# Kernel optimization log

Hardware: AMD Instinct MI355X
Metric: run time of the kernel (lower is better)

The kernel has to match this reference:

```python
import jax, jax.numpy as jnp
import numpy as np

B, N, D = 4096, 20, 256
MAX_STEPS = int(N * 1.5)  # exploration_ratio = 1.5


def setup_inputs() -> dict:
    key = jax.random.key(0)
    ks = jax.random.split(key, 9)
    s = 1.0 / np.sqrt(D)
    u = lambda k, shape: jax.random.uniform(k, shape, jnp.float32, -s, s)
    return {
        "node_emb": jax.random.normal(ks[0], (B, N, D), jnp.float32),
        "mask": jnp.ones((B, N), jnp.bool_),  # present in signature, unused by forward
        "W_ih": u(ks[1], (4 * D, D)),
        "W_hh": u(ks[2], (4 * D, D)),
        "b_ih": u(ks[3], (4 * D,)),
        "b_hh": u(ks[4], (4 * D,)),
        "attn_w": u(ks[5], (D, D)),
        "attn_b": u(ks[6], (D,)),
        "done_w": u(ks[7], (D,)),
        "done_b": u(ks[8], ()),
        "revisit_penalty": jnp.float32(-0.05),
        "greedy": 1,
    }


def reference(node_emb, mask, W_ih, W_hh, b_ih, b_hh, attn_w, attn_b, done_w, done_b, revisit_penalty, greedy):
    Bx, Nx, Dx = node_emb.shape
    aB = jnp.arange(Bx)
    aN = jnp.arange(Nx)
    scale = 1.0 / jnp.sqrt(jnp.float32(Dx))
    keys = node_emb @ attn_w.T + attn_b  # [B, N, D], loop-invariant

    def step(carry, t):
        h, c, inp, visited, unique, complete, first = carry
        # LSTMCell (PyTorch gate order i, f, g, o)
        gates = inp @ W_ih.T + b_ih + h @ W_hh.T + b_hh
        i, f, g, o = jnp.split(gates, 4, axis=1)
        c2 = jax.nn.sigmoid(f) * c + jax.nn.sigmoid(i) * jnp.tanh(g)
        h2 = jax.nn.sigmoid(o) * jnp.tanh(c2)
        # done predictor (greedy: complete when sigmoid > 0.5)
        done_p = jax.nn.sigmoid(h2 @ done_w + done_b)  # [B]
        eligible = (~complete) & (unique >= Nx) & (t >= Nx)
        complete2 = complete | (eligible & (done_p > 0.5))
        # pointer scores
        scores = jnp.einsum('bd,bnd->bn', h2, keys) * scale
        rev = ((~complete2) & (unique < Nx))[:, None] & visited
        scores = jnp.where(rev, revisit_penalty, scores)
        scores = jnp.where(complete2[:, None], jnp.float32(-1e9), scores)
        scores = jnp.where(complete2[:, None] & (aN[None, :] == first[:, None]), jnp.float32(100.0), scores)
        probs = jax.nn.softmax(scores, axis=1)
        choice = jnp.argmax(probs, axis=1).astype(jnp.int32)
        curr = jnp.where(complete2, first, choice)
        logp = jnp.log(probs[aB, curr] + 1e-10)
        first2 = jnp.where(t == 0, curr, first)
        newly = (~complete2) & (~visited[aB, curr])
        unique2 = unique + newly.astype(jnp.int32)
        visited2 = visited.at[aB, curr].set(visited[aB, curr] | (~complete2))
        inp2 = node_emb[aB, curr]
        return (h2, c2, inp2, visited2, unique2, complete2, first2), (curr, logp)

    init = (
        jnp.zeros((Bx, Dx), jnp.float32),
        jnp.zeros((Bx, Dx), jnp.float32),
        node_emb.mean(axis=1),
        jnp.zeros((Bx, Nx), jnp.bool_),
        jnp.zeros((Bx,), jnp.int32),
        jnp.zeros((Bx,), jnp.bool_),
        jnp.zeros((Bx,), jnp.int32),
    )
    carry, (tours_t, logps_t) = jax.lax.scan(step, init, jnp.arange(MAX_STEPS))
    complete, first = carry[5], carry[6]
    # step == max_steps: incomplete tours are closed at first_node, log-prob 0
    final_node = jnp.where(~complete, first, jnp.int32(0))
    tours = jnp.concatenate([tours_t.T, final_node[:, None]], axis=1)   # [B, MAX_STEPS+1]
    logps = jnp.concatenate([logps_t.T, jnp.zeros((Bx, 1), jnp.float32)], axis=1)
    return tours, logps
```

## Files before the change

kernel.cpp:

```cpp
#include <hip/hip_runtime.h>
#include <cstdint>
#include <cstddef>

#define NB   4096
#define NN   20
#define DD   256
#define TST  30
#define RPB  16
#define NTHR 512
#define SCALE 0.0625f

__device__ __forceinline__ float sigf(float x) {
    return 1.0f / (1.0f + expf(-x));
}

__global__ __launch_bounds__(256) void keys_gemm(
    const float* __restrict__ A, const float* __restrict__ W,
    const float* __restrict__ bias, float* __restrict__ C)
{
    __shared__ float As[64][33];
    __shared__ float Bs[64][33];
    const int bm = blockIdx.x * 64;
    const int bn = blockIdx.y * 64;
    const int t  = threadIdx.x;
    const int tm = t >> 4, tn = t & 15;
    const int sr = t >> 3;
    const int sk = (t & 7) << 2;
    float acc[4][4] = {};
    for (int k0 = 0; k0 < DD; k0 += 32) {
        __syncthreads();
#pragma unroll
        for (int p = 0; p < 2; ++p) {
            const int r = sr + p * 32;
            const float4 va = *(const float4*)&A[(size_t)(bm + r) * DD + k0 + sk];
            As[r][sk] = va.x; As[r][sk + 1] = va.y; As[r][sk + 2] = va.z; As[r][sk + 3] = va.w;
            const float4 vb = *(const float4*)&W[(size_t)(bn + r) * DD + k0 + sk];
            Bs[r][sk] = vb.x; Bs[r][sk + 1] = vb.y; Bs[r][sk + 2] = vb.z; Bs[r][sk + 3] = vb.w;
        }
        __syncthreads();
#pragma unroll
        for (int k = 0; k < 32; ++k) {
            float a[4], b[4];
#pragma unroll
            for (int i = 0; i < 4; ++i) a[i] = As[tm * 4 + i][k];
#pragma unroll
            for (int j = 0; j < 4; ++j) b[j] = Bs[tn * 4 + j][k];
#pragma unroll
            for (int i = 0; i < 4; ++i)
#pragma unroll
                for (int j = 0; j < 4; ++j)
                    acc[i][j] = fmaf(a[i], b[j], acc[i][j]);
        }
    }
#pragma unroll
    for (int i = 0; i < 4; ++i) {
        const int row = bm + tm * 4 + i;
#pragma unroll
        for (int j = 0; j < 4; ++j) {
            const int col = bn + tn * 4 + j;
            C[(size_t)row * DD + col] = acc[i][j] + bias[col];
        }
    }
}

__global__ __launch_bounds__(NTHR, 1) void decode(
    const float* __restrict__ ne,
    const float* __restrict__ wih,
    const float* __restrict__ whh,
    const float* __restrict__ bih,
    const float* __restrict__ bhh,
    const float* __restrict__ dwv,
    const float* __restrict__ dbp,
    const float* __restrict__ rpp,
    const float* __restrict__ keys,
    float* __restrict__ out)
{
    __shared__ float xcat[RPB][512];
    __shared__ float gates[RPB][1024];

    const int t    = threadIdx.x;
    const int b0   = blockIdx.x * RPB;
    const int lane = t & 63;
    const int w    = t >> 6;
    const int rg   = t >> 8;
    const int kh   = (t >> 7) & 1;
    const int cg   = t & 127;
    const int mg   = t >> 7;
    const int ni3  = t & 127;
    const int xb   = kh << 8;
    const int rbase = rg << 3;

    const float done_b = dbp[0];
    const float rp     = rpp[0];

    float bsv[8];
#pragma unroll
    for (int g = 0; g < 8; ++g) {
        const int j = (g >> 1) * 256 + ((g & 1) << 7) + ni3;
        bsv[g] = bih[j] + bhh[j];
    }
    const float4 dv = *(const float4*)&dwv[lane * 4];

    const float* Wb = kh ? whh : wih;
    const float* wp[8];
#pragma unroll
    for (int j = 0; j < 8; ++j) wp[j] = Wb + (size_t)(cg + (j << 7)) * DD;

    for (int idx = t; idx < RPB * 256; idx += NTHR)
        xcat[idx >> 8][256 + (idx & 255)] = 0.0f;
#pragma unroll
    for (int rr = 0; rr < 2; ++rr) {
        const int r = w * 2 + rr;
        const int b = b0 + r;
        float sx = 0.f, sy = 0.f, sz = 0.f, sw = 0.f;
        for (int n = 0; n < NN; ++n) {
            const float4 v = *(const float4*)&ne[((size_t)b * NN + n) * DD + lane * 4];
            sx += v.x; sy += v.y; sz += v.z; sw += v.w;
        }
        float4 m4;
        m4.x = sx / 20.0f; m4.y = sy / 20.0f; m4.z = sz / 20.0f; m4.w = sw / 20.0f;
        *(float4*)&xcat[r][lane * 4] = m4;
    }

    float creg[4][2] = {};
    unsigned vm[2] = {0u, 0u};
    int un[2] = {0, 0}, fn[2] = {0, 0}, cm[2] = {0, 0};

    for (int step = 0; step < TST; ++step) {
        __syncthreads();

        float acc[8][8] = {};
#pragma unroll 2
        for (int kc = 0; kc < 64; ++kc) {
            float4 wv[8];
#pragma unroll
            for (int j = 0; j < 8; ++j)
                wv[j] = *(const float4*)(wp[j] + (kc << 2));
#pragma unroll
            for (int r = 0; r < 8; ++r) {
                const float4 x4 = *(const float4*)&xcat[rbase + r][xb + (kc << 2)];
#pragma unroll
                for (int j = 0; j < 8; ++j) {
                    acc[r][j] = fmaf(x4.x, wv[j].x, acc[r][j]);
                    acc[r][j] = fmaf(x4.y, wv[j].y, acc[r][j]);
                    acc[r][j] = fmaf(x4.z, wv[j].z, acc[r][j]);
                    acc[r][j] = fmaf(x4.w, wv[j].w, acc[r][j]);
                }
            }
        }

        if (kh == 0) {
#pragma unroll
            for (int r = 0; r < 8; ++r)
#pragma unroll
                for (int j = 0; j < 8; ++j)
                    gates[rbase + r][cg + (j << 7)] = acc[r][j];
        }
        __syncthreads();
        if (kh == 1) {
#pragma unroll
            for (int r = 0; r < 8; ++r)
#pragma unroll
                for (int j = 0; j < 8; ++j)
                    gates[rbase + r][cg + (j << 7)] += acc[r][j];
        }
        __syncthreads();

#pragma unroll
        for (int i = 0; i < 4; ++i) {
            const int r = (mg << 2) + i;
#pragma unroll
            for (int dd = 0; dd < 2; ++dd) {
                const int d = ni3 + (dd << 7);
                const float gi = gates[r][d]       + bsv[0 + dd];
                const float gf = gates[r][d + 256] + bsv[2 + dd];
                const float gg = gates[r][d + 512] + bsv[4 + dd];
                const float go = gates[r][d + 768] + bsv[6 + dd];
                const float co = creg[i][dd];
                const float cn = sigf(gf) * co + sigf(gi) * tanhf(gg);
                const float hn = sigf(go) * tanhf(cn);
                creg[i][dd] = cn;
                xcat[r][256 + d] = hn;
            }
        }
        __syncthreads();

#pragma unroll
        for (int rr = 0; rr < 2; ++rr) {
            const int r = w * 2 + rr;
            const int b = b0 + r;
            const float4 h4 = *(const float4*)&xcat[r][256 + lane * 4];

            float pd = h4.x * dv.x + h4.y * dv.y + h4.z * dv.z + h4.w * dv.w;
#pragma unroll
            for (int o = 32; o >= 1; o >>= 1) pd += __shfl_xor(pd, o);

            float ps[NN];
            const float* kb = keys + (size_t)b * NN * DD + lane * 4;
#pragma unroll
            for (int n = 0; n < NN; ++n) {
                const float4 kv = *(const float4*)(kb + n * DD);
                ps[n] = h4.x * kv.x + h4.y * kv.y + h4.z * kv.z + h4.w * kv.w;
            }
#pragma unroll
            for (int n = 0; n < NN; ++n) {
                float v = ps[n];
#pragma unroll
                for (int o = 32; o >= 1; o >>= 1) v += __shfl_xor(v, o);
                ps[n] = v;
            }

            const float dprob = 1.0f / (1.0f + expf(-(pd + done_b)));
            const int elig = (!cm[rr]) && (un[rr] >= NN) && (step >= NN);
            const int cm2  = cm[rr] || (elig && (dprob > 0.5f));

            float sv[NN];
#pragma unroll
            for (int n = 0; n < NN; ++n) {
                float s = ps[n] * SCALE;
                if ((!cm2) && (un[rr] < NN) && ((vm[rr] >> n) & 1u)) s = rp;
                if (cm2) s = (n == fn[rr]) ? 100.0f : -1e9f;
                sv[n] = s;
            }
            float m = sv[0];
#pragma unroll
            for (int n = 1; n < NN; ++n) m = fmaxf(m, sv[n]);
            float e[NN]; float se = 0.0f;
#pragma unroll
            for (int n = 0; n < NN; ++n) { e[n] = expf(sv[n] - m); se += e[n]; }
            float pmax = e[0] / se; int idx = 0;
#pragma unroll
            for (int n = 1; n < NN; ++n) {
                const float pn = e[n] / se;
                if (pn > pmax) { pmax = pn; idx = n; }
            }
            const int curr  = cm2 ? fn[rr] : idx;
            const float pc  = cm2 ? 1.0f : pmax;
            const float lp  = logf(pc + 1e-10f);

            if (step == 0) fn[rr] = curr;
            const int newly = (!cm2) && !((vm[rr] >> curr) & 1u);
            if (!cm2) vm[rr] |= (1u << curr);
            un[rr] += newly;
            cm[rr] = cm2;

            if (lane == 0) {
                out[(size_t)b * (TST + 1) + step] = (float)curr;
                out[(size_t)NB * (TST + 1) + (size_t)b * (TST + 1) + step] = lp;
            }
            const float4 nv = *(const float4*)&ne[((size_t)b * NN + curr) * DD + lane * 4];
            *(float4*)&xcat[r][lane * 4] = nv;
        }
    }

#pragma unroll
    for (int rr = 0; rr < 2; ++rr) {
        const int b = b0 + w * 2 + rr;
        if (lane == 0) {
            out[(size_t)b * (TST + 1) + TST] = cm[rr] ? 0.0f : (float)fn[rr];
            out[(size_t)NB * (TST + 1) + (size_t)b * (TST + 1) + TST] = 0.0f;
        }
    }
}

extern "C" void kernel_launch(void* const* d_in, const int* in_sizes, int n_in,
                              void* d_out, int out_size, void* d_ws, size_t ws_size,
                              hipStream_t stream) {
    (void)in_sizes; (void)n_in; (void)out_size;
    const float* ne  = (const float*)d_in[0];
    const float* wih = (const float*)d_in[2];
    const float* whh = (const float*)d_in[3];
    const float* bih = (const float*)d_in[4];
    const float* bhh = (const float*)d_in[5];
    const float* aw  = (const float*)d_in[6];
    const float* ab  = (const float*)d_in[7];
    const float* dw  = (const float*)d_in[8];
    const float* db  = (const float*)d_in[9];
    const float* rp  = (const float*)d_in[10];
    float* out  = (float*)d_out;
    float* keys = (float*)d_ws;
    if (ws_size < (size_t)NB * NN * DD * sizeof(float)) return;

    keys_gemm<<<dim3((NB * NN) / 64, DD / 64), 256, 0, stream>>>(ne, aw, ab, keys);
    decode<<<dim3(NB / RPB), NTHR, 0, stream>>>(ne, wih, whh, bih, bhh, dw, db, rp, keys, out);
}
```

Before: 4.665 ms.

## Double decode block threads and software-pipeline LSTM weight loads

Raises the decode block from 512 to 1024 threads, so each thread computes 8 rows by 4 gate columns instead of 8 by 8, and each wave handles one batch row in the pointer and softmax phase instead of two. The weight loads in the gate GEMM loop are double-buffered, with the next k-chunk fetched while the current one is multiplied. The goal is more latency hiding and less register pressure per thread. In exchange the min-blocks hint is dropped, and the weights are re-read from global or L2 memory every step, so more threads issue those loads per block.

```diff
diff --git a/kernel.cpp b/kernel.cpp
--- a/kernel.cpp
+++ b/kernel.cpp
@@ -7,7 +7,7 @@
 #define DD   256
 #define TST  30
 #define RPB  16
-#define NTHR 512
+#define NTHR 1024
 #define SCALE 0.0625f
 
 __device__ __forceinline__ float sigf(float x) {
@@ -63,7 +63,7 @@
     }
 }
 
-__global__ __launch_bounds__(NTHR, 1) void decode(
+__global__ __launch_bounds__(NTHR) void decode(
     const float* __restrict__ ne,
     const float* __restrict__ wih,
     const float* __restrict__ whh,
@@ -82,36 +82,31 @@
     const int b0   = blockIdx.x * RPB;
     const int lane = t & 63;
     const int w    = t >> 6;
-    const int rg   = t >> 8;
-    const int kh   = (t >> 7) & 1;
-    const int cg   = t & 127;
-    const int mg   = t >> 7;
-    const int ni3  = t & 127;
+    const int rg   = t >> 9;
+    const int kh   = (t >> 8) & 1;
+    const int cg   = t & 255;
     const int xb   = kh << 8;
     const int rbase = rg << 3;
+    const int rq   = t >> 8;
+    const int dl   = t & 255;
 
     const float done_b = dbp[0];
     const float rp     = rpp[0];
 
-    float bsv[8];
-#pragma unroll
-    for (int g = 0; g < 8; ++g) {
-        const int j = (g >> 1) * 256 + ((g & 1) << 7) + ni3;
-        bsv[g] = bih[j] + bhh[j];
-    }
+    float bsv[4];
+#pragma unroll
+    for (int g = 0; g < 4; ++g) bsv[g] = bih[g * 256 + dl] + bhh[g * 256 + dl];
     const float4 dv = *(const float4*)&dwv[lane * 4];
 
     const float* Wb = kh ? whh : wih;
-    const float* wp[8];
-#pragma unroll
-    for (int j = 0; j < 8; ++j) wp[j] = Wb + (size_t)(cg + (j << 7)) * DD;
+    const float* wp[4];
+#pragma unroll
+    for (int j = 0; j < 4; ++j) wp[j] = Wb + (size_t)(cg + (j << 8)) * DD;
 
     for (int idx = t; idx < RPB * 256; idx += NTHR)
         xcat[idx >> 8][256 + (idx & 255)] = 0.0f;
-#pragma unroll
-    for (int rr = 0; rr < 2; ++rr) {
-        const int r = w * 2 + rr;
-        const int b = b0 + r;
+    {
+        const int b = b0 + w;
         float sx = 0.f, sy = 0.f, sz = 0.f, sw = 0.f;
         for (int n = 0; n < NN; ++n) {
             const float4 v = *(const float4*)&ne[((size_t)b * NN + n) * DD + lane * 4];
@@ -119,75 +114,86 @@
         }
         float4 m4;
         m4.x = sx / 20.0f; m4.y = sy / 20.0f; m4.z = sz / 20.0f; m4.w = sw / 20.0f;
-        *(float4*)&xcat[r][lane * 4] = m4;
-    }
-
-    float creg[4][2] = {};
-    unsigned vm[2] = {0u, 0u};
-    int un[2] = {0, 0}, fn[2] = {0, 0}, cm[2] = {0, 0};
+        *(float4*)&xcat[w][lane * 4] = m4;
+    }
+
+    float creg[4] = {};
+    unsigned vm = 0u;
+    int un = 0, fn = 0, cm = 0;
+
+    auto ldw = [&](int kc, float4 (&wv)[4]) {
+#pragma unroll
+        for (int j = 0; j < 4; ++j)
+            wv[j] = *(const float4*)(wp[j] + (kc << 2));
+    };
 
     for (int step = 0; step < TST; ++step) {
         __syncthreads();
 
-        float acc[8][8] = {};
-#pragma unroll 2
-        for (int kc = 0; kc < 64; ++kc) {
-            float4 wv[8];
-#pragma unroll
-            for (int j = 0; j < 8; ++j)
-                wv[j] = *(const float4*)(wp[j] + (kc << 2));
+        float acc[8][4] = {};
+        float4 wA[4], wB[4];
+        ldw(0, wA);
+#pragma unroll 1
+        for (int kc = 0; kc < 64; kc += 2) {
+            ldw(kc + 1, wB);
 #pragma unroll
             for (int r = 0; r < 8; ++r) {
                 const float4 x4 = *(const float4*)&xcat[rbase + r][xb + (kc << 2)];
 #pragma unroll
-                for (int j = 0; j < 8; ++j) {
-                    acc[r][j] = fmaf(x4.x, wv[j].x, acc[r][j]);
-                    acc[r][j] = fmaf(x4.y, wv[j].y, acc[r][j]);
-                    acc[r][j] = fmaf(x4.z, wv[j].z, acc[r][j]);
-                    acc[r][j] = fmaf(x4.w, wv[j].w, acc[r][j]);
+                for (int j = 0; j < 4; ++j) {
+                    acc[r][j] = fmaf(x4.x, wA[j].x, acc[r][j]);
+                    acc[r][j] = fmaf(x4.y, wA[j].y, acc[r][j]);
+                    acc[r][j] = fmaf(x4.z, wA[j].z, acc[r][j]);
+                    acc[r][j] = fmaf(x4.w, wA[j].w, acc[r][j]);
                 }
             }
+            if (kc + 2 < 64) ldw(kc + 2, wA);
+#pragma unroll
+            for (int r = 0; r < 8; ++r) {
+                const float4 x4 = *(const float4*)&xcat[rbase + r][xb + ((kc + 1) << 2)];
+#pragma unroll
+                for (int j = 0; j < 4; ++j) {
+                    acc[r][j] = fmaf(x4.x, wB[j].x, acc[r][j]);
+                    acc[r][j] = fmaf(x4.y, wB[j].y, acc[r][j]);
+                    acc[r][j] = fmaf(x4.z, wB[j].z, acc[r][j]);
+                    acc[r][j] = fmaf(x4.w, wB[j].w, acc[r][j]);
+                }
+            }
         }
 
         if (kh == 0) {
 #pragma unroll
             for (int r = 0; r < 8; ++r)
 #pragma unroll
-                for (int j = 0; j < 8; ++j)
-                    gates[rbase + r][cg + (j << 7)] = acc[r][j];
+                for (int j = 0; j < 4; ++j)
+                    gates[rbase + r][cg + (j << 8)] = acc[r][j];
         }
         __syncthreads();
         if (kh == 1) {
 #pragma unroll
             for (int r = 0; r < 8; ++r)
 #pragma unroll
-                for (int j = 0; j < 8; ++j)
-                    gates[rbase + r][cg + (j << 7)] += acc[r][j];
+                for (int j = 0; j < 4; ++j)
+                    gates[rbase + r][cg + (j << 8)] += acc[r][j];
         }
         __syncthreads();
 
 #pragma unroll
         for (int i = 0; i < 4; ++i) {
-            const int r = (mg << 2) + i;
-#pragma unroll
-            for (int dd = 0; dd < 2; ++dd) {
-                const int d = ni3 + (dd << 7);
-                const float gi = gates[r][d]       + bsv[0 + dd];
-                const float gf = gates[r][d + 256] + bsv[2 + dd];
-                const float gg = gates[r][d + 512] + bsv[4 + dd];
-                const float go = gates[r][d + 768] + bsv[6 + dd];
-                const float co = creg[i][dd];
-                const float cn = sigf(gf) * co + sigf(gi) * tanhf(gg);
-                const float hn = sigf(go) * tanhf(cn);
-                creg[i][dd] = cn;
-                xcat[r][256 + d] = hn;
-            }
-        }
-        __syncthreads();
-
-#pragma unroll
-        for (int rr = 0; rr < 2; ++rr) {
-            const int r = w * 2 + rr;
+            const int r = (rq << 2) + i;
+            const float gi = gates[r][dl]       + bsv[0];
+            const float gf = gates[r][dl + 256] + bsv[1];
+            const float gg = gates[r][dl + 512] + bsv[2];
+            const float go = gates[r][dl + 768] + bsv[3];
+            const float cn = sigf(gf) * creg[i] + sigf(gi) * tanhf(gg);
+            const float hn = sigf(go) * tanhf(cn);
+            creg[i] = cn;
+            xcat[r][256 + dl] = hn;
+        }
+        __syncthreads();
+
+        {
+            const int r = w;
             const int b = b0 + r;
             const float4 h4 = *(const float4*)&xcat[r][256 + lane * 4];
 
@@ -211,15 +217,15 @@
             }
 
             const float dprob = 1.0f / (1.0f + expf(-(pd + done_b)));
-            const int elig = (!cm[rr]) && (un[rr] >= NN) && (step >= NN);
-            const int cm2  = cm[rr] || (elig && (dprob > 0.5f));
+            const int elig = (!cm) && (un >= NN) && (step >= NN);
+            const int cm2  = cm || (elig && (dprob > 0.5f));
 
             float sv[NN];
 #pragma unroll
             for (int n = 0; n < NN; ++n) {
                 float s = ps[n] * SCALE;
-                if ((!cm2) && (un[rr] < NN) && ((vm[rr] >> n) & 1u)) s = rp;
-                if (cm2) s = (n == fn[rr]) ? 100.0f : -1e9f;
+                if ((!cm2) && (un < NN) && ((vm >> n) & 1u)) s = rp;
+                if (cm2) s = (n == fn) ? 100.0f : -1e9f;
                 sv[n] = s;
             }
             float m = sv[0];
@@ -234,15 +240,15 @@
                 const float pn = e[n] / se;
                 if (pn > pmax) { pmax = pn; idx = n; }
             }
-            const int curr  = cm2 ? fn[rr] : idx;
+            const int curr  = cm2 ? fn : idx;
             const float pc  = cm2 ? 1.0f : pmax;
             const float lp  = logf(pc + 1e-10f);
 
-            if (step == 0) fn[rr] = curr;
-            const int newly = (!cm2) && !((vm[rr] >> curr) & 1u);
-            if (!cm2) vm[rr] |= (1u << curr);
-            un[rr] += newly;
-            cm[rr] = cm2;
+            if (step == 0) fn = curr;
+            const int newly = (!cm2) && !((vm >> curr) & 1u);
+            if (!cm2) vm |= (1u << curr);
+            un += newly;
+            cm = cm2;
 
             if (lane == 0) {
                 out[(size_t)b * (TST + 1) + step] = (float)curr;
@@ -253,13 +259,10 @@
         }
     }
 
-#pragma unroll
-    for (int rr = 0; rr < 2; ++rr) {
-        const int b = b0 + w * 2 + rr;
-        if (lane == 0) {
-            out[(size_t)b * (TST + 1) + TST] = cm[rr] ? 0.0f : (float)fn[rr];
-            out[(size_t)NB * (TST + 1) + (size_t)b * (TST + 1) + TST] = 0.0f;
-        }
+    if (lane == 0) {
+        const int b = b0 + w;
+        out[(size_t)b * (TST + 1) + TST] = cm ? 0.0f : (float)fn;
+        out[(size_t)NB * (TST + 1) + (size_t)b * (TST + 1) + TST] = 0.0f;
     }
 }
 
```

Measured after the change: 7.928 ms. 69.9% more time.
